# Performance work log

Hardware: AMD Instinct MI355X
Metric: run time of the kernel (lower is better)

Reference implementation:

```python
import jax, jax.numpy as jnp
import numpy as np

N = 100000
E = 1600000
IN_F = 128
OUT_F = 128
EPS = 1e-12


def setup_inputs() -> dict:
    key = jax.random.key(0)
    k1, k2, k3, k4, k5, k6 = jax.random.split(key, 6)
    x = jax.random.normal(k1, (N, IN_F), dtype=jnp.float32)
    rows = jnp.sort(jax.random.randint(k2, (E,), 0, N, dtype=jnp.int32))
    cols = jax.random.randint(k3, (E,), 0, N, dtype=jnp.int32)
    vals = jax.random.uniform(k4, (E,), dtype=jnp.float32)
    # nn.Linear(2*in_features, out_features): W is [out, 2*in], b is [out]
    bound = 1.0 / np.sqrt(2 * IN_F)
    W = jax.random.uniform(k5, (OUT_F, 2 * IN_F), dtype=jnp.float32, minval=-bound, maxval=bound)
    b = jax.random.uniform(k6, (OUT_F,), dtype=jnp.float32, minval=-bound, maxval=bound)
    return {"x": x, "rows": rows, "cols": cols, "vals": vals, "W": W, "b": b}


def reference(x, rows, cols, vals, W, b):
    # spmm(adj, x): gather source-node features, scale by edge weight,
    # segment-sum into destination rows.
    gathered = vals[:, None] * x[cols]                      # [E, in]
    neighbor = jax.ops.segment_sum(gathered, rows, num_segments=N)  # [N, in]
    combined = jnp.concatenate([x, neighbor], axis=1)       # [N, 2*in]
    out = combined @ W.T + b                                # [N, out]
    # F.normalize(out, p=2, dim=1): divide by max(||row||_2, eps)
    norm = jnp.sqrt(jnp.sum(out * out, axis=1, keepdims=True))
    return out / jnp.maximum(norm, EPS)
```

## Files before the change

kernel.cpp:

```cpp
#include <hip/hip_runtime.h>
#include <hip/hip_bf16.h>


typedef __bf16 bf16x8_t __attribute__((ext_vector_type(8)));
typedef float f32x4_t __attribute__((ext_vector_type(4)));
typedef float f32x2_t __attribute__((ext_vector_type(2)));
typedef unsigned int u32x4_t __attribute__((ext_vector_type(4)));

#define DESC_CAP 512
#define RING_D   4

__device__ __forceinline__ unsigned int f32_to_bf16(float f) {
    unsigned int u = __float_as_uint(f);
    unsigned int r = u + 0x7fffu + ((u >> 16) & 1u);
    return r >> 16;
}
__device__ __forceinline__ unsigned int pack2(float a, float b) {
    return f32_to_bf16(a) | (f32_to_bf16(b) << 16);
}
__device__ __forceinline__ float bflo(unsigned int p) { return __uint_as_float(p << 16); }
__device__ __forceinline__ float bfhi(unsigned int p) { return __uint_as_float(p & 0xffff0000u); }

__device__ __forceinline__ void gload_lds16(const char* g, void* l) {
    auto gp = reinterpret_cast<__attribute__((address_space(1))) unsigned int*>(
        reinterpret_cast<uintptr_t>(g));
    auto lp = reinterpret_cast<__attribute__((address_space(3))) unsigned int*>(
        reinterpret_cast<uintptr_t>(l));
    __builtin_amdgcn_global_load_lds(gp, lp, 16, 0, 0);
}

__global__ void prep_kernel(const float* __restrict__ x, uint4* __restrict__ xb4,
                            const int* __restrict__ rows, int* __restrict__ row_ptr,
                            const float* __restrict__ W, uint4* __restrict__ Wf,
                            int Nn, int Ee, int xcast_blks, int rowptr_blks) {
    int blk = blockIdx.x;
    if (blk < xcast_blks) {
        int i = blk * 256 + threadIdx.x;
        if (i < Nn * 16) {
            const f32x4_t* xf = (const f32x4_t*)x;
            f32x4_t f0 = __builtin_nontemporal_load(&xf[(size_t)i * 2]);
            f32x4_t f1 = __builtin_nontemporal_load(&xf[(size_t)i * 2 + 1]);
            u32x4_t o;
            o.x = pack2(f0.x, f0.y); o.y = pack2(f0.z, f0.w);
            o.z = pack2(f1.x, f1.y); o.w = pack2(f1.z, f1.w);
            __builtin_nontemporal_store(o, (u32x4_t*)&xb4[i]);
        }
    } else if (blk < xcast_blks + rowptr_blks) {
        int n = (blk - xcast_blks) * 256 + threadIdx.x;
        if (n <= Nn) {
            int lo = 0, hi = Ee;
            while (lo < hi) {
                int mid = (lo + hi) >> 1;
                if (rows[mid] < n) lo = mid + 1; else hi = mid;
            }
            row_ptr[n] = lo;
        }
    } else {
        int i = (blk - xcast_blks - rowptr_blks) * 256 + threadIdx.x;
        int lane = i & 63, ks = (i >> 6) & 7, t = i >> 9;
        int row = t * 16 + (lane & 15);
        int col = ks * 32 + (lane >> 4) * 8;
        const float* p = W + (size_t)row * 256 + col;
        uint4 o;
        o.x = pack2(p[0], p[1]); o.y = pack2(p[2], p[3]);
        o.z = pack2(p[4], p[5]); o.w = pack2(p[6], p[7]);
        Wf[i] = o;
    }
}

__global__ void __launch_bounds__(256, 6)
fused_kernel(const int* __restrict__ row_ptr,
             const int* __restrict__ cols,
             const float* __restrict__ vals,
             const char* __restrict__ xbB,
             const bf16x8_t* __restrict__ Wf,
             const float* __restrict__ b,
             float* __restrict__ out, int Nn) {
    __shared__ uint4 ring[4][RING_D][64];
    __shared__ int   cLDS[DESC_CAP];
    __shared__ float vLDS[DESC_CAP];
    __shared__ uint4 nbLDS[16 * 17];
    __shared__ float __attribute__((aligned(16))) sqLDS[16][4];

    int lane = threadIdx.x & 63;
    int w    = threadIdx.x >> 6;
    int r0   = blockIdx.x * 16;

    int eLo = row_ptr[r0];
    int eHi = row_ptr[min(r0 + 16, Nn)];
    int cnt = eHi - eLo;
    bool big = cnt > DESC_CAP;

    if (!big) {
        for (int i = threadIdx.x; i < cnt; i += 256) {
            cLDS[i] = __builtin_nontemporal_load(&cols[eLo + i]);
            vLDS[i] = __builtin_nontemporal_load(&vals[eLo + i]);
        }
        if (threadIdx.x == 0 && cnt == 0) { cLDS[0] = 0; vLDS[0] = 0.f; }
    }
    __syncthreads();

    {
        int h = lane >> 4;
        int l = lane & 15;
        int node = w * 4 + h;
        int n = r0 + node;
        int nn = min(n, Nn - 1);
        int start = row_ptr[nn], end = row_ptr[nn + 1];
        if (n >= Nn) end = start;
        unsigned loff = (unsigned)l << 4;

        f32x2_t a0 = {0.f, 0.f}, a1 = {0.f, 0.f}, a2 = {0.f, 0.f}, a3 = {0.f, 0.f};

#define ACC1(p, V) {                                                        \
        f32x2_t vv2 = {(V), (V)};                                           \
        f32x2_t t0 = {bflo((p).x), bfhi((p).x)};                            \
        f32x2_t t1 = {bflo((p).y), bfhi((p).y)};                            \
        f32x2_t t2 = {bflo((p).z), bfhi((p).z)};                            \
        f32x2_t t3 = {bflo((p).w), bfhi((p).w)};                            \
        a0 += vv2 * t0; a1 += vv2 * t1; a2 += vv2 * t2; a3 += vv2 * t3;     \
}

        if (!big) {
            int deg   = end - start;
            int degm1 = deg - 1;
            int soff  = start - eLo;
            int tgw   = deg;
            tgw = max(tgw, __shfl_xor(tgw, 16, 64));
            tgw = max(tgw, __shfl_xor(tgw, 32, 64));

#pragma unroll
            for (int s = 0; s < RING_D; ++s) {
                int idx = max(soff + min(s, degm1), 0);
                int c = cLDS[idx];
                gload_lds16(xbB + (((unsigned)c << 8) | loff), &ring[w][s][0]);
            }

            for (int g = 0; g < tgw; ++g) {
                asm volatile("s_waitcnt vmcnt(3)" ::: "memory");
                uint4 P = ring[w][g & (RING_D - 1)][lane];
                int idxN = max(soff + min(g + RING_D, degm1), 0);
                int cN   = cLDS[idxN];
                int idxV = max(soff + min(g, degm1), 0);
                float vv = vLDS[idxV];
                if (g >= deg) vv = 0.f;
                asm volatile("s_waitcnt lgkmcnt(0)" ::: "memory");
                gload_lds16(xbB + (((unsigned)cN << 8) | loff),
                            &ring[w][g & (RING_D - 1)][0]);
                ACC1(P, vv);
            }
        } else {
#define EDGE4B(E, C0, C1, C2, C3, V0, V1, V2, V3)                               \
            {                                                                   \
                int q0 = min((E), end - 1),     q1 = min((E) + 1, end - 1);     \
                int q2 = min((E) + 2, end - 1), q3 = min((E) + 3, end - 1);     \
                C0 = cols[q0]; C1 = cols[q1]; C2 = cols[q2]; C3 = cols[q3];     \
                V0 = ((E)     < end) ? vals[q0] : 0.f;                          \
                V1 = ((E) + 1 < end) ? vals[q1] : 0.f;                          \
                V2 = ((E) + 2 < end) ? vals[q2] : 0.f;                          \
                V3 = ((E) + 3 < end) ? vals[q3] : 0.f;                          \
            }
            int e = start;
            int c0 = 0, c1 = 0, c2 = 0, c3 = 0;
            float v0 = 0.f, v1 = 0.f, v2 = 0.f, v3 = 0.f;
            if (e < end) EDGE4B(e, c0, c1, c2, c3, v0, v1, v2, v3);
            while (e < end) {
                int en = e + 4;
                int d0 = 0, d1 = 0, d2 = 0, d3 = 0;
                float w0 = 0.f, w1 = 0.f, w2 = 0.f, w3 = 0.f;
                if (en < end) EDGE4B(en, d0, d1, d2, d3, w0, w1, w2, w3);
                uint4 p0 = *(const uint4*)(xbB + (((unsigned)c0 << 8) | loff));
                uint4 p1 = *(const uint4*)(xbB + (((unsigned)c1 << 8) | loff));
                uint4 p2 = *(const uint4*)(xbB + (((unsigned)c2 << 8) | loff));
                uint4 p3 = *(const uint4*)(xbB + (((unsigned)c3 << 8) | loff));
                ACC1(p0, v0); ACC1(p1, v1); ACC1(p2, v2); ACC1(p3, v3);
                c0 = d0; c1 = d1; c2 = d2; c3 = d3;
                v0 = w0; v1 = w1; v2 = w2; v3 = w3;
                e = en;
            }
#undef EDGE4B
        }
#undef ACC1

        uint4 o;
        o.x = pack2(a0.x, a0.y); o.y = pack2(a1.x, a1.y);
        o.z = pack2(a2.x, a2.y); o.w = pack2(a3.x, a3.y);
        nbLDS[node * 17 + l] = o;
    }
    __syncthreads();

    int m    = lane & 15;
    int quad = lane >> 4;

    int arow = min(r0 + m, Nn - 1);
    const bf16x8_t* Ax = (const bf16x8_t*)(xbB + (size_t)arow * 256);

    bf16x8_t a[8];
#pragma unroll
    for (int ks = 0; ks < 4; ++ks) a[ks] = Ax[ks * 4 + quad];
#pragma unroll
    for (int ks = 0; ks < 4; ++ks)
        a[4 + ks] = *(const bf16x8_t*)&nbLDS[m * 17 + ks * 4 + quad];

    f32x4_t acc[2];
    float bc[2];
#pragma unroll
    for (int j = 0; j < 2; ++j) {
        int t = w * 2 + j;
        acc[j] = (f32x4_t){0.f, 0.f, 0.f, 0.f};
        bc[j]  = b[t * 16 + m];
#pragma unroll
        for (int ks = 0; ks < 8; ++ks) {
            acc[j] = __builtin_amdgcn_mfma_f32_16x16x32_bf16(
                a[ks], Wf[(t * 8 + ks) * 64 + lane], acc[j], 0, 0, 0);
        }
    }

    float sq[4] = {0.f, 0.f, 0.f, 0.f};
#pragma unroll
    for (int j = 0; j < 2; ++j)
#pragma unroll
        for (int r = 0; r < 4; ++r) {
            float u = acc[j][r] + bc[j];
            sq[r] += u * u;
        }
#pragma unroll
    for (int off = 1; off <= 8; off <<= 1) {
#pragma unroll
        for (int r = 0; r < 4; ++r) sq[r] += __shfl_xor(sq[r], off, 64);
    }
    if (m == 0) {
#pragma unroll
        for (int r = 0; r < 4; ++r) sqLDS[quad * 4 + r][w] = sq[r];
    }
    __syncthreads();

    float scale[4];
#pragma unroll
    for (int r = 0; r < 4; ++r) {
        const float4 q4 = *(const float4*)sqLDS[quad * 4 + r];
        float tot = q4.x + q4.y + q4.z + q4.w;
        scale[r] = 1.f / fmaxf(sqrtf(tot), 1e-12f);
    }

#pragma unroll
    for (int r = 0; r < 4; ++r) {
        int row = r0 + quad * 4 + r;
        if (row < Nn) {
            float* orow = out + (size_t)row * 128;
#pragma unroll
            for (int j = 0; j < 2; ++j) {
                int t = w * 2 + j;
                __builtin_nontemporal_store((acc[j][r] + bc[j]) * scale[r],
                                            &orow[t * 16 + m]);
            }
        }
    }
}

extern "C" void kernel_launch(void* const* d_in, const int* in_sizes, int n_in,
                              void* d_out, int out_size, void* d_ws, size_t ws_size,
                              hipStream_t stream) {
    const float* x    = (const float*)d_in[0];
    const int*   rows = (const int*)  d_in[1];
    const int*   cols = (const int*)  d_in[2];
    const float* vals = (const float*)d_in[3];
    const float* W    = (const float*)d_in[4];
    const float* b    = (const float*)d_in[5];
    float*       out  = (float*)d_out;

    const int Nn = in_sizes[0] / 128;
    const int Ee = in_sizes[1];

    char*  ws      = (char*)d_ws;
    int*   row_ptr = (int*)ws;
    uint4* Wf      = (uint4*)(ws + 448 * 1024);
    uint4* xb      = (uint4*)(ws + 640 * 1024);

    const int xcast_blks  = (Nn * 16 + 255) / 256;
    const int rowptr_blks = (Nn + 1 + 255) / 256;
    const int wcast_blks  = 16;

    prep_kernel<<<xcast_blks + rowptr_blks + wcast_blks, 256, 0, stream>>>(
        x, xb, rows, row_ptr, W, Wf, Nn, Ee, xcast_blks, rowptr_blks);
    fused_kernel<<<(Nn + 15) / 16, 256, 0, stream>>>(
        row_ptr, cols, vals, (const char*)xb,
        (const bf16x8_t*)Wf, b, out, Nn);
}
```

Before: 191.8 us.

## Process gather per wavefront over edge range with segmented row accumulation

Replaces the per-node 16-lane gather, which used a global_load_lds ring buffer, with a scheme where each wavefront walks the edges of its 4 rows. Every lane loads one 4-byte slice of the 256-byte bf16 row, prefetching 8 edges deep in registers. Each edge descriptor in LDS now packs the local row id into the top bits of the column index, and a row's partial sum is flushed to LDS when the row id changes. This removes the load imbalance from padding to the largest degree among the 4 nodes a wave handles and drops the LDS staging ring. In exchange it issues 4-byte instead of 16-byte gathers, adds an LDS zeroing pass and a binary search per edge, and limits column indices to 28 bits.

```diff
diff --git a/kernel.cpp b/kernel.cpp
--- a/kernel.cpp
+++ b/kernel.cpp
@@ -8,7 +8,7 @@
 typedef unsigned int u32x4_t __attribute__((ext_vector_type(4)));
 
 #define DESC_CAP 512
-#define RING_D   4
+#define RING_D   8
 
 __device__ __forceinline__ unsigned int f32_to_bf16(float f) {
     unsigned int u = __float_as_uint(f);
@@ -20,14 +20,6 @@
 }
 __device__ __forceinline__ float bflo(unsigned int p) { return __uint_as_float(p << 16); }
 __device__ __forceinline__ float bfhi(unsigned int p) { return __uint_as_float(p & 0xffff0000u); }
-
-__device__ __forceinline__ void gload_lds16(const char* g, void* l) {
-    auto gp = reinterpret_cast<__attribute__((address_space(1))) unsigned int*>(
-        reinterpret_cast<uintptr_t>(g));
-    auto lp = reinterpret_cast<__attribute__((address_space(3))) unsigned int*>(
-        reinterpret_cast<uintptr_t>(l));
-    __builtin_amdgcn_global_load_lds(gp, lp, 16, 0, 0);
-}
 
 __global__ void prep_kernel(const float* __restrict__ x, uint4* __restrict__ xb4,
                             const int* __restrict__ rows, int* __restrict__ row_ptr,
@@ -76,9 +68,8 @@
              const bf16x8_t* __restrict__ Wf,
              const float* __restrict__ b,
              float* __restrict__ out, int Nn) {
-    __shared__ uint4 ring[4][RING_D][64];
-    __shared__ int   cLDS[DESC_CAP];
-    __shared__ float vLDS[DESC_CAP];
+    __shared__ int   rpS[17];
+    __shared__ uint2 cvLDS[DESC_CAP];
     __shared__ uint4 nbLDS[16 * 17];
     __shared__ float __attribute__((aligned(16))) sqLDS[16][4];
 
@@ -86,21 +77,82 @@
     int w    = threadIdx.x >> 6;
     int r0   = blockIdx.x * 16;
 
-    int eLo = row_ptr[r0];
-    int eHi = row_ptr[min(r0 + 16, Nn)];
+    if (threadIdx.x < 17)
+        rpS[threadIdx.x] = row_ptr[min(r0 + (int)threadIdx.x, Nn)];
+    __syncthreads();
+
+    int eLo = rpS[0], eHi = rpS[16];
     int cnt = eHi - eLo;
     bool big = cnt > DESC_CAP;
 
     if (!big) {
         for (int i = threadIdx.x; i < cnt; i += 256) {
-            cLDS[i] = __builtin_nontemporal_load(&cols[eLo + i]);
-            vLDS[i] = __builtin_nontemporal_load(&vals[eLo + i]);
-        }
-        if (threadIdx.x == 0 && cnt == 0) { cLDS[0] = 0; vLDS[0] = 0.f; }
+            int e = eLo + i;
+            int c = __builtin_nontemporal_load(&cols[e]);
+            float v = __builtin_nontemporal_load(&vals[e]);
+            int d = (e >= rpS[8]) ? 8 : 0;
+            d += (e >= rpS[d + 4]) ? 4 : 0;
+            d += (e >= rpS[d + 2]) ? 2 : 0;
+            d += (e >= rpS[d + 1]) ? 1 : 0;
+            uint2 cv;
+            cv.x = (unsigned)c | ((unsigned)d << 28);
+            cv.y = __float_as_uint(v);
+            cvLDS[i] = cv;
+        }
+    }
+    {
+        unsigned* nz = (unsigned*)nbLDS;
+        for (int i = threadIdx.x; i < 16 * 17 * 4; i += 256) nz[i] = 0u;
     }
     __syncthreads();
 
-    {
+    if (!big) {
+        int wLo = __builtin_amdgcn_readfirstlane(rpS[w * 4]     - eLo);
+        int wHi = __builtin_amdgcn_readfirstlane(rpS[w * 4 + 4] - eLo);
+        int nEd = wHi - wLo;
+        if (nEd > 0) {
+            unsigned lane2 = (unsigned)lane << 2;
+            int wHiM1 = wHi - 1;
+            unsigned* nbW = (unsigned*)nbLDS;
+
+            unsigned P[RING_D];
+            uint2    cv[RING_D];
+#pragma unroll
+            for (int d = 0; d < RING_D; ++d) {
+                int kd = min(wLo + d, wHiM1);
+                cv[d] = cvLDS[kd];
+                unsigned voff = ((cv[d].x & 0x0FFFFFFFu) << 8) | lane2;
+                P[d] = *(const unsigned*)(xbB + voff);
+            }
+            int cur = (int)(cv[0].x >> 28);
+            float ax = 0.f, ay = 0.f;
+
+            int nit = (nEd + RING_D - 1) / RING_D;
+            int k0 = wLo;
+            for (int it = 0; it < nit; ++it, k0 += RING_D) {
+#pragma unroll
+                for (int d = 0; d < RING_D; ++d) {
+                    int k = k0 + d;
+                    uint2 cvk = cv[d];
+                    int dk = (int)(cvk.x >> 28);
+                    if (dk != cur) {
+                        nbW[cur * 68 + lane] = pack2(ax, ay);
+                        ax = 0.f; ay = 0.f;
+                        cur = dk;
+                    }
+                    float vv = (k < wHi) ? __uint_as_float(cvk.y) : 0.f;
+                    unsigned Pd = P[d];
+                    ax += vv * bflo(Pd);
+                    ay += vv * bfhi(Pd);
+                    uint2 cvn = cvLDS[min(k + RING_D, wHiM1)];
+                    unsigned voff = ((cvn.x & 0x0FFFFFFFu) << 8) | lane2;
+                    P[d] = *(const unsigned*)(xbB + voff);
+                    cv[d] = cvn;
+                }
+            }
+            nbW[cur * 68 + lane] = pack2(ax, ay);
+        }
+    } else {
         int h = lane >> 4;
         int l = lane & 15;
         int node = w * 4 + h;
@@ -120,68 +172,36 @@
         f32x2_t t3 = {bflo((p).w), bfhi((p).w)};                            \
         a0 += vv2 * t0; a1 += vv2 * t1; a2 += vv2 * t2; a3 += vv2 * t3;     \
 }
-
-        if (!big) {
-            int deg   = end - start;
-            int degm1 = deg - 1;
-            int soff  = start - eLo;
-            int tgw   = deg;
-            tgw = max(tgw, __shfl_xor(tgw, 16, 64));
-            tgw = max(tgw, __shfl_xor(tgw, 32, 64));
-
-#pragma unroll
-            for (int s = 0; s < RING_D; ++s) {
-                int idx = max(soff + min(s, degm1), 0);
-                int c = cLDS[idx];
-                gload_lds16(xbB + (((unsigned)c << 8) | loff), &ring[w][s][0]);
-            }
-
-            for (int g = 0; g < tgw; ++g) {
-                asm volatile("s_waitcnt vmcnt(3)" ::: "memory");
-                uint4 P = ring[w][g & (RING_D - 1)][lane];
-                int idxN = max(soff + min(g + RING_D, degm1), 0);
-                int cN   = cLDS[idxN];
-                int idxV = max(soff + min(g, degm1), 0);
-                float vv = vLDS[idxV];
-                if (g >= deg) vv = 0.f;
-                asm volatile("s_waitcnt lgkmcnt(0)" ::: "memory");
-                gload_lds16(xbB + (((unsigned)cN << 8) | loff),
-                            &ring[w][g & (RING_D - 1)][0]);
-                ACC1(P, vv);
-            }
-        } else {
 #define EDGE4B(E, C0, C1, C2, C3, V0, V1, V2, V3)                               \
-            {                                                                   \
-                int q0 = min((E), end - 1),     q1 = min((E) + 1, end - 1);     \
-                int q2 = min((E) + 2, end - 1), q3 = min((E) + 3, end - 1);     \
-                C0 = cols[q0]; C1 = cols[q1]; C2 = cols[q2]; C3 = cols[q3];     \
-                V0 = ((E)     < end) ? vals[q0] : 0.f;                          \
-                V1 = ((E) + 1 < end) ? vals[q1] : 0.f;                          \
-                V2 = ((E) + 2 < end) ? vals[q2] : 0.f;                          \
-                V3 = ((E) + 3 < end) ? vals[q3] : 0.f;                          \
-            }
-            int e = start;
-            int c0 = 0, c1 = 0, c2 = 0, c3 = 0;
-            float v0 = 0.f, v1 = 0.f, v2 = 0.f, v3 = 0.f;
-            if (e < end) EDGE4B(e, c0, c1, c2, c3, v0, v1, v2, v3);
-            while (e < end) {
-                int en = e + 4;
-                int d0 = 0, d1 = 0, d2 = 0, d3 = 0;
-                float w0 = 0.f, w1 = 0.f, w2 = 0.f, w3 = 0.f;
-                if (en < end) EDGE4B(en, d0, d1, d2, d3, w0, w1, w2, w3);
-                uint4 p0 = *(const uint4*)(xbB + (((unsigned)c0 << 8) | loff));
-                uint4 p1 = *(const uint4*)(xbB + (((unsigned)c1 << 8) | loff));
-                uint4 p2 = *(const uint4*)(xbB + (((unsigned)c2 << 8) | loff));
-                uint4 p3 = *(const uint4*)(xbB + (((unsigned)c3 << 8) | loff));
-                ACC1(p0, v0); ACC1(p1, v1); ACC1(p2, v2); ACC1(p3, v3);
-                c0 = d0; c1 = d1; c2 = d2; c3 = d3;
-                v0 = w0; v1 = w1; v2 = w2; v3 = w3;
-                e = en;
-            }
+        {                                                                       \
+            int q0 = min((E), end - 1),     q1 = min((E) + 1, end - 1);         \
+            int q2 = min((E) + 2, end - 1), q3 = min((E) + 3, end - 1);         \
+            C0 = cols[q0]; C1 = cols[q1]; C2 = cols[q2]; C3 = cols[q3];         \
+            V0 = ((E)     < end) ? vals[q0] : 0.f;                              \
+            V1 = ((E) + 1 < end) ? vals[q1] : 0.f;                              \
+            V2 = ((E) + 2 < end) ? vals[q2] : 0.f;                              \
+            V3 = ((E) + 3 < end) ? vals[q3] : 0.f;                              \
+        }
+        int e = start;
+        int c0 = 0, c1 = 0, c2 = 0, c3 = 0;
+        float v0 = 0.f, v1 = 0.f, v2 = 0.f, v3 = 0.f;
+        if (e < end) EDGE4B(e, c0, c1, c2, c3, v0, v1, v2, v3);
+        while (e < end) {
+            int en = e + 4;
+            int d0 = 0, d1 = 0, d2 = 0, d3 = 0;
+            float w0 = 0.f, w1 = 0.f, w2 = 0.f, w3 = 0.f;
+            if (en < end) EDGE4B(en, d0, d1, d2, d3, w0, w1, w2, w3);
+            uint4 p0 = *(const uint4*)(xbB + (((unsigned)c0 << 8) | loff));
+            uint4 p1 = *(const uint4*)(xbB + (((unsigned)c1 << 8) | loff));
+            uint4 p2 = *(const uint4*)(xbB + (((unsigned)c2 << 8) | loff));
+            uint4 p3 = *(const uint4*)(xbB + (((unsigned)c3 << 8) | loff));
+            ACC1(p0, v0); ACC1(p1, v1); ACC1(p2, v2); ACC1(p3, v3);
+            c0 = d0; c1 = d1; c2 = d2; c3 = d3;
+            v0 = w0; v1 = w1; v2 = w2; v3 = w3;
+            e = en;
+        }
 #undef EDGE4B
-        }
 #undef ACC1
-
         uint4 o;
         o.x = pack2(a0.x, a0.y); o.y = pack2(a1.x, a1.y);
         o.z = pack2(a2.x, a2.y); o.w = pack2(a3.x, a3.y);
```

New measurement: 194.7 us. Within noise of the previous version (+1.5%).
